# Optimization experiments

Measured on AMD Instinct MI355X. Metric: run time of the kernel, lower is better.

## Reference

```python
import jax, jax.numpy as jnp
import numpy as np

B, C, L = 8, 2048, 256          # batch, seq (EEG channels), feature length
E = 3 * L                        # embed_dim = 768 (fused QKV width)
H = 4                            # attention heads
D = E // (3 * H)                 # head_dim = 64
SCALE = 8.0                      # hardcoded in the module (== sqrt(D) here)


def _layer_norm(x, gamma, beta, eps=1e-5):
    mu = jnp.mean(x, axis=-1, keepdims=True)
    var = jnp.var(x, axis=-1, keepdims=True)
    return (x - mu) * jax.lax.rsqrt(var + eps) * gamma + beta


def setup_inputs() -> dict:
    key = jax.random.key(0)
    ks = jax.random.split(key, 5)
    x = jax.random.normal(ks[0], (B, C, L), dtype=jnp.float32)
    # layers_1: Linear(L -> E) + LayerNorm(E)
    W1 = jax.random.normal(ks[1], (L, E), dtype=jnp.float32) / np.sqrt(L)
    b1 = jnp.zeros((E,), dtype=jnp.float32)
    g1 = jnp.ones((E,), dtype=jnp.float32)
    beta1 = jnp.zeros((E,), dtype=jnp.float32)
    # layers_2: Linear(L -> L) + LayerNorm(L)
    W2 = jax.random.normal(ks[2], (L, L), dtype=jnp.float32) / np.sqrt(L)
    b2 = jnp.zeros((L,), dtype=jnp.float32)
    g2 = jnp.ones((L,), dtype=jnp.float32)
    beta2 = jnp.zeros((L,), dtype=jnp.float32)
    return {"x": x, "W1": W1, "b1": b1, "g1": g1, "beta1": beta1,
            "W2": W2, "b2": b2, "g2": g2, "beta2": beta2}


def reference(x, W1, b1, g1, beta1, W2, b2, g2, beta2):
    b, c, _ = x.shape
    # layers_1 (dropout is identity in eval mode)
    y = _layer_norm(x @ W1 + b1, g1, beta1)                     # [b, c, E]
    qkv = y.reshape(b, c, 3, H, D).transpose(2, 0, 3, 1, 4)     # [3, b, H, c, D]
    q, k, v = qkv[0], qkv[1], qkv[2]
    attn = jax.nn.softmax(jnp.einsum('bhqd,bhkd->bhqk', q, k) / SCALE, axis=-1)
    o = jnp.einsum('bhqk,bhkd->bhqd', attn, v)                  # [b, H, c, D]
    o = o.transpose(0, 2, 1, 3).reshape(b, c, H * D)            # [b, c, L]
    # layers_2 + residual
    z = _layer_norm(o @ W2 + b2, g2, beta2) + x
    return z
```

## Files before the change

### kernel.cpp

```cpp
#include <hip/hip_runtime.h>
#include <hip/hip_bf16.h>

#define B_ 8
#define C_ 2048
#define L_ 256
#define E_ 768
#define H_ 4
#define D_ 64
#define M_ (B_*C_)

typedef __attribute__((ext_vector_type(8))) short short8v;
typedef __attribute__((ext_vector_type(4))) short short4v;
typedef __attribute__((ext_vector_type(4))) float f32x4;

__device__ __forceinline__ short f2bf(float f) {
  union { float f; unsigned u; } v; v.f = f;
  unsigned r = v.u + 0x7FFFu + ((v.u >> 16) & 1u);
  return (short)(r >> 16);
}
__device__ __forceinline__ float bf2f(short s) {
  union { unsigned u; float f; } v; v.u = ((unsigned)(unsigned short)s) << 16;
  return v.f;
}
__device__ __forceinline__ unsigned cvtpk(float a, float b) {
  unsigned r;
  asm("v_cvt_pk_bf16_f32 %0, %1, %2" : "=v"(r) : "v"(a), "v"(b));
  return r;
}
__device__ __forceinline__ float exp2x(float x) {
  float r;
  asm("v_exp_f32 %0, %1" : "=v"(r) : "v"(x));
  return r;
}

__device__ __forceinline__ void gll16(const void* g, void* l) {
  __builtin_amdgcn_global_load_lds(
      (const __attribute__((address_space(1))) unsigned int*)g,
      (__attribute__((address_space(3))) unsigned int*)l, 16, 0, 0);
}

__global__ __launch_bounds__(256) void transpose_w_kernel(const float* __restrict__ W,
                                                          short* __restrict__ Wt,
                                                          int K, int N) {
  __shared__ float ld[32][33];
  const int k0 = blockIdx.x * 32, n0 = blockIdx.y * 32;
  const int tx = threadIdx.x & 31, ty = threadIdx.x >> 5;
  #pragma unroll
  for (int j = 0; j < 4; ++j)
    ld[ty + j*8][tx] = W[(size_t)(k0 + ty + j*8) * N + n0 + tx];
  __syncthreads();
  const int r  = threadIdx.x >> 3;
  const int c0 = (threadIdx.x & 7) * 4;
  short4v o;
  o[0]=f2bf(ld[c0+0][r]); o[1]=f2bf(ld[c0+1][r]);
  o[2]=f2bf(ld[c0+2][r]); o[3]=f2bf(ld[c0+3][r]);
  *(short4v*)(Wt + (size_t)(n0 + r) * K + k0 + c0) = o;
}

__global__ __launch_bounds__(256) void gemm1_mfma_kernel(
    const float* __restrict__ x, const short* __restrict__ W1t,
    const float* __restrict__ b1, short* __restrict__ y1) {
  __shared__ short As[128*72];
  __shared__ short Bs[128*72];
  const int tid = threadIdx.x;
  const int w = tid >> 6, l = tid & 63, lo = l & 15, hi = l >> 4;
  const int wr = w >> 1, wc = w & 1;
  const int m0 = blockIdx.x * 128, n0 = blockIdx.y * 128;

  f32x4 acc[4][4];
  #pragma unroll
  for (int m = 0; m < 4; ++m)
    #pragma unroll
    for (int n = 0; n < 4; ++n) acc[m][n] = (f32x4){0.f,0.f,0.f,0.f};

  for (int kt = 0; kt < 4; ++kt) {
    __syncthreads();
    #pragma unroll
    for (int i = 0; i < 4; ++i) {
      int id = tid + i * 256;
      int row = id >> 3, k8 = (id & 7) * 8;
      const float* ap = x + (size_t)(m0 + row) * 256 + kt*64 + k8;
      float4 a0 = ((const float4*)ap)[0], a1 = ((const float4*)ap)[1];
      uint4 pk;
      pk.x = cvtpk(a0.x, a0.y); pk.y = cvtpk(a0.z, a0.w);
      pk.z = cvtpk(a1.x, a1.y); pk.w = cvtpk(a1.z, a1.w);
      *(uint4*)&As[row*72 + k8] = pk;
      *(short8v*)&Bs[row*72 + k8] =
          *(const short8v*)(W1t + (size_t)(n0 + row) * 256 + kt*64 + k8);
    }
    __syncthreads();
    #pragma unroll
    for (int kk = 0; kk < 2; ++kk) {
      short8v af[4], bf[4];
      #pragma unroll
      for (int m = 0; m < 4; ++m)
        af[m] = *(short8v*)&As[(wr*64 + m*16 + lo)*72 + kk*32 + hi*8];
      #pragma unroll
      for (int n = 0; n < 4; ++n)
        bf[n] = *(short8v*)&Bs[(wc*64 + n*16 + lo)*72 + kk*32 + hi*8];
      #pragma unroll
      for (int m = 0; m < 4; ++m)
        #pragma unroll
        for (int n = 0; n < 4; ++n)
          acc[m][n] = __builtin_amdgcn_mfma_f32_16x16x32_bf16(af[m], bf[n], acc[m][n], 0,0,0);
    }
  }

  float bb[4];
  #pragma unroll
  for (int n = 0; n < 4; ++n) bb[n] = b1[n0 + wc*64 + n*16 + lo];
  #pragma unroll
  for (int m = 0; m < 4; ++m) {
    const int gr = m0 + wr*64 + m*16 + hi*4;
    #pragma unroll
    for (int r = 0; r < 4; ++r) {
      short* yp = y1 + (size_t)(gr + r) * E_ + n0 + wc*64;
      #pragma unroll
      for (int n = 0; n < 4; ++n)
        yp[n*16 + lo] = f2bf(acc[m][n][r] + bb[n]);
    }
  }
}

__global__ __launch_bounds__(256) void ln1_kernel(
    const short* __restrict__ y1, const float* __restrict__ g1,
    const float* __restrict__ be1,
    short* __restrict__ Qg, short* __restrict__ Kg, short* __restrict__ Vtg) {
  __shared__ float mu_s[64], rs_s[64];
  __shared__ short Vlds[64][264];
  const int tid = threadIdx.x;
  const int w = tid >> 6, l = tid & 63;
  const int b = blockIdx.x >> 5;
  const int c0 = (blockIdx.x & 31) * 64;
  const size_t rowbase = (size_t)b * C_ + c0;

  for (int rr = w*16; rr < w*16 + 16; ++rr) {
    const short* yr = y1 + (rowbase + rr) * E_ + l * 12;
    float s = 0.f, s2 = 0.f;
    #pragma unroll
    for (int j = 0; j < 3; ++j) {
      short4v v = *(const short4v*)(yr + j*4);
      #pragma unroll
      for (int t = 0; t < 4; ++t) { float f = bf2f(v[t]); s += f; s2 += f*f; }
    }
    #pragma unroll
    for (int off = 1; off < 64; off <<= 1) {
      s  += __shfl_xor(s, off);
      s2 += __shfl_xor(s2, off);
    }
    if (l == 0) {
      float mu = s * (1.f / E_);
      float var = s2 * (1.f / E_) - mu * mu;
      mu_s[rr] = mu;
      rs_s[rr] = rsqrtf(var + 1e-5f);
    }
  }
  __syncthreads();

  {
    const int chunk = tid & 63, e0 = chunk * 8;
    float gg[8], ee[8];
    #pragma unroll
    for (int j = 0; j < 8; ++j) { gg[j] = g1[e0+j]; ee[j] = be1[e0+j]; }
    const int isQ = (e0 < 256);
    const int eb  = isQ ? e0 : e0 - 256;
    const int h = eb >> 6, d0 = eb & 63;
    short* dstQ = Qg + ((size_t)(b*H_ + h) * C_ + c0) * D_ + d0;
    short* dstK = Kg + ((size_t)(b*H_ + h) * C_ + c0) * D_;
    const float qs = isQ ? 0.18033688011f : 1.f;
    for (int rg = 0; rg < 16; ++rg) {
      int rr = rg*4 + (tid >> 6);
      short8v v = *(const short8v*)(y1 + (rowbase + rr) * E_ + e0);
      float mu = mu_s[rr], rs = rs_s[rr];
      short8v o;
      #pragma unroll
      for (int j = 0; j < 8; ++j)
        o[j] = f2bf(((bf2f(v[j]) - mu) * rs * gg[j] + ee[j]) * qs);
      if (isQ) *(short8v*)(dstQ + (size_t)rr * D_) = o;
      else     *(short8v*)(dstK + (size_t)rr * D_ + ((((d0>>3) ^ (rr&7)) << 3))) = o;
    }
  }
  {
    const int chunk = tid & 31, e0 = 512 + chunk * 8;
    float gg[8], ee[8];
    #pragma unroll
    for (int j = 0; j < 8; ++j) { gg[j] = g1[e0+j]; ee[j] = be1[e0+j]; }
    for (int rg = 0; rg < 8; ++rg) {
      int rr = rg*8 + (tid >> 5);
      short8v v = *(const short8v*)(y1 + (rowbase + rr) * E_ + e0);
      float mu = mu_s[rr], rs = rs_s[rr];
      short8v o;
      #pragma unroll
      for (int j = 0; j < 8; ++j)
        o[j] = f2bf((bf2f(v[j]) - mu) * rs * gg[j] + ee[j]);
      *(short8v*)&Vlds[rr][chunk * 8] = o;
    }
  }
  __syncthreads();
  {
    const int h = tid >> 6, d = tid & 63;
    short* dst = Vtg + ((size_t)(b*H_ + h) * D_ + d) * C_ + c0;
    #pragma unroll
    for (int c8 = 0; c8 < 8; ++c8) {
      short8v vv;
      #pragma unroll
      for (int j = 0; j < 8; ++j) vv[j] = Vlds[c8*8 + j][tid];
      *(short8v*)(dst + ((c8 ^ (d&7)) << 3)) = vv;
    }
  }
}

__global__ __launch_bounds__(512, 4) void attn_mfma_kernel(
    const short* __restrict__ Qg, const short* __restrict__ Kg,
    const short* __restrict__ Vtg, short* __restrict__ ob) {
  __shared__ short Ks[3][4096];
  __shared__ short Vs[3][4096];
  __shared__ short Ps[8][1024];
  const int tid = threadIdx.x;
  const int w  = tid >> 6;
  const int l  = tid & 63, lo = l & 15, hi = l >> 4;
  const int sw = lo & 7;
  const int bh = blockIdx.x, qt = blockIdx.y;
  const size_t hd = (size_t)bh * (C_ * D_);
  const int q0 = qt * 128 + w * 16;

  const short8v bq0 = *(const short8v*)(Qg + hd + (size_t)(q0+lo)*D_ + hi*8);
  const short8v bq1 = *(const short8v*)(Qg + hd + (size_t)(q0+lo)*D_ + 32 + hi*8);

  short8v ones;
  #pragma unroll
  for (int j = 0; j < 8; ++j) ones[j] = (short)0x3F80;

  const short* Ktile = Kg + hd;
  const short* Vrow  = Vtg + hd;
  const int kOff = w*512 + l*8;
  const size_t vOff = (size_t)(w*8 + (l>>3)) * C_ + (l&7)*8;

  f32x4 Oacc[4] = {{0,0,0,0},{0,0,0,0},{0,0,0,0},{0,0,0,0}};
  f32x4 Lacc = {0.f, 0.f, 0.f, 0.f};
  const f32x4 zero4 = {0.f, 0.f, 0.f, 0.f};
  short* Pw = &Ps[w][0];

  gll16(Ktile + kOff, &Ks[0][w*512]);
  gll16(Vrow + vOff,  &Vs[0][w*512]);

  int cur = 0, nxt = 1;
  for (int kt = 0; kt < 32; ++kt) {
    asm volatile("s_waitcnt vmcnt(0)" ::: "memory");
    __builtin_amdgcn_s_barrier();
    if (kt != 31) {
      const short* kn = Ktile + (size_t)(kt+1) * 4096;
      const short* vn = Vrow  + (size_t)(kt+1) * 64;
      gll16(kn + kOff, &Ks[nxt][w*512]);
      gll16(vn + vOff, &Vs[nxt][w*512]);
    }
    const short* Kc = &Ks[cur][0];
    const short* Vc = &Vs[cur][0];

    f32x4 st[4];
    __builtin_amdgcn_s_setprio(1);
    #pragma unroll
    for (int mt = 0; mt < 4; ++mt) {
      short8v ka = *(const short8v*)&Kc[(mt*16 + lo)*64 + ((hi ^ sw) << 3)];
      short8v kb = *(const short8v*)&Kc[(mt*16 + lo)*64 + (((4 + hi) ^ sw) << 3)];
      f32x4 z = __builtin_amdgcn_mfma_f32_16x16x32_bf16(ka, bq0, zero4, 0, 0, 0);
      st[mt]  = __builtin_amdgcn_mfma_f32_16x16x32_bf16(kb, bq1, z, 0, 0, 0);
    }
    __builtin_amdgcn_s_setprio(0);

    float ps[16];
    #pragma unroll
    for (int mt = 0; mt < 4; ++mt)
      #pragma unroll
      for (int r = 0; r < 4; ++r)
        ps[mt*4 + r] = exp2x(st[mt][r]);

    #pragma unroll
    for (int mt = 0; mt < 4; ++mt) {
      uint2 pk;
      pk.x = cvtpk(ps[mt*4+0], ps[mt*4+1]);
      pk.y = cvtpk(ps[mt*4+2], ps[mt*4+3]);
      *(uint2*)&Pw[lo*64 + ((((mt<<1) + (hi>>1)) ^ sw) << 3) + ((hi&1) << 2)] = pk;
    }
    asm volatile("s_waitcnt lgkmcnt(0)" ::: "memory");

    short8v pa0 = *(short8v*)&Pw[lo*64 + ((hi ^ sw) << 3)];
    short8v pa1 = *(short8v*)&Pw[lo*64 + (((4 + hi) ^ sw) << 3)];
    __builtin_amdgcn_s_setprio(1);
    Lacc = __builtin_amdgcn_mfma_f32_16x16x32_bf16(pa0, ones, Lacc, 0, 0, 0);
    Lacc = __builtin_amdgcn_mfma_f32_16x16x32_bf16(pa1, ones, Lacc, 0, 0, 0);
    #pragma unroll
    for (int nt = 0; nt < 4; ++nt) {
      short8v vb0 = *(const short8v*)&Vc[(nt*16 + lo)*64 + ((hi ^ sw) << 3)];
      short8v vb1 = *(const short8v*)&Vc[(nt*16 + lo)*64 + (((4 + hi) ^ sw) << 3)];
      Oacc[nt] = __builtin_amdgcn_mfma_f32_16x16x32_bf16(pa0, vb0, Oacc[nt], 0,0,0);
      Oacc[nt] = __builtin_amdgcn_mfma_f32_16x16x32_bf16(pa1, vb1, Oacc[nt], 0,0,0);
    }
    __builtin_amdgcn_s_setprio(0);
    cur = nxt;
    nxt = (nxt == 2) ? 0 : nxt + 1;
  }

  float invL[4];
  #pragma unroll
  for (int r = 0; r < 4; ++r) invL[r] = 1.f / Lacc[r];
  const int b = bh >> 2, h = bh & 3;
  short* obp = ob + ((size_t)b * C_ + q0) * L_ + h * D_;
  #pragma unroll
  for (int nt = 0; nt < 4; ++nt)
    #pragma unroll
    for (int r = 0; r < 4; ++r)
      obp[(hi*4 + r) * L_ + nt*16 + lo] = f2bf(Oacc[nt][r] * invL[r]);
}

__global__ __launch_bounds__(256) void gemm2_ln_mfma_kernel(
    const short* __restrict__ ob, const short* __restrict__ W2t,
    const float* __restrict__ b2, const float* __restrict__ g2,
    const float* __restrict__ be2, const float* __restrict__ x,
    float* __restrict__ out) {
  __shared__ short As[64*72];
  __shared__ short Bs[256*72];
  __shared__ float2 red[2][2][32];
  const int tid = threadIdx.x;
  const int w = tid >> 6, l = tid & 63, lo = l & 15, hi = l >> 4;
  const int wr = w >> 1, wc = w & 1;
  const int m0 = blockIdx.x * 64;

  f32x4 acc[2][8];
  #pragma unroll
  for (int m = 0; m < 2; ++m)
    #pragma unroll
    for (int n = 0; n < 8; ++n) acc[m][n] = (f32x4){0.f,0.f,0.f,0.f};

  for (int kt = 0; kt < 4; ++kt) {
    __syncthreads();
    #pragma unroll
    for (int i = 0; i < 2; ++i) {
      int id = tid + i * 256;
      int row = id >> 3, k8 = (id & 7) * 8;
      *(short8v*)&As[row*72 + k8] =
          *(const short8v*)(ob + (size_t)(m0 + row) * 256 + kt*64 + k8);
    }
    #pragma unroll
    for (int i = 0; i < 8; ++i) {
      int id = tid + i * 256;
      int row = id >> 3, k8 = (id & 7) * 8;
      *(short8v*)&Bs[row*72 + k8] =
          *(const short8v*)(W2t + (size_t)row * 256 + kt*64 + k8);
    }
    __syncthreads();
    #pragma unroll
    for (int kk = 0; kk < 2; ++kk) {
      short8v af[2], bf[8];
      #pragma unroll
      for (int m = 0; m < 2; ++m)
        af[m] = *(short8v*)&As[(wr*32 + m*16 + lo)*72 + kk*32 + hi*8];
      #pragma unroll
      for (int n = 0; n < 8; ++n)
        bf[n] = *(short8v*)&Bs[(wc*128 + n*16 + lo)*72 + kk*32 + hi*8];
      #pragma unroll
      for (int m = 0; m < 2; ++m)
        #pragma unroll
        for (int n = 0; n < 8; ++n)
          acc[m][n] = __builtin_amdgcn_mfma_f32_16x16x32_bf16(af[m], bf[n], acc[m][n], 0,0,0);
    }
  }

  float bb[8], gg[8], ee[8];
  #pragma unroll
  for (int n = 0; n < 8; ++n) {
    int col = wc*128 + n*16 + lo;
    bb[n] = b2[col]; gg[n] = g2[col]; ee[n] = be2[col];
  }
  float ps[2][4], pq[2][4];
  #pragma unroll
  for (int m = 0; m < 2; ++m)
    #pragma unroll
    for (int r = 0; r < 4; ++r) {
      float s = 0.f, s2 = 0.f;
      #pragma unroll
      for (int n = 0; n < 8; ++n) {
        float v = acc[m][n][r] + bb[n];
        acc[m][n][r] = v;
        s += v; s2 += v*v;
      }
      ps[m][r] = s; pq[m][r] = s2;
    }
  #pragma unroll
  for (int off = 1; off < 16; off <<= 1)
    #pragma unroll
    for (int m = 0; m < 2; ++m)
      #pragma unroll
      for (int r = 0; r < 4; ++r) {
        ps[m][r] += __shfl_xor(ps[m][r], off);
        pq[m][r] += __shfl_xor(pq[m][r], off);
      }
  if (lo == 0)
    #pragma unroll
    for (int m = 0; m < 2; ++m)
      #pragma unroll
      for (int r = 0; r < 4; ++r)
        red[wr][wc][m*16 + hi*4 + r] = make_float2(ps[m][r], pq[m][r]);
  __syncthreads();

  #pragma unroll
  for (int m = 0; m < 2; ++m)
    #pragma unroll
    for (int r = 0; r < 4; ++r) {
      float2 t0 = red[wr][0][m*16 + hi*4 + r];
      float2 t1 = red[wr][1][m*16 + hi*4 + r];
      float s = t0.x + t1.x, s2 = t0.y + t1.y;
      float mu  = s * (1.f / L_);
      float var = s2 * (1.f / L_) - mu * mu;
      float rs  = rsqrtf(var + 1e-5f);
      const int grow = m0 + wr*32 + m*16 + hi*4 + r;
      const float* xr = x + (size_t)grow * L_ + wc*128;
      float* orow = out + (size_t)grow * L_ + wc*128;
      #pragma unroll
      for (int n = 0; n < 8; ++n)
        orow[n*16 + lo] = (acc[m][n][r] - mu) * rs * gg[n] + ee[n] + xr[n*16 + lo];
    }
}

extern "C" void kernel_launch(void* const* d_in, const int* in_sizes, int n_in,
                              void* d_out, int out_size, void* d_ws, size_t ws_size,
                              hipStream_t stream) {
  const float* x   = (const float*)d_in[0];
  const float* W1  = (const float*)d_in[1];
  const float* b1  = (const float*)d_in[2];
  const float* g1  = (const float*)d_in[3];
  const float* be1 = (const float*)d_in[4];
  const float* W2  = (const float*)d_in[5];
  const float* b2  = (const float*)d_in[6];
  const float* g2  = (const float*)d_in[7];
  const float* be2 = (const float*)d_in[8];
  float* out = (float*)d_out;

  const size_t HDSZ = (size_t)B_ * H_ * C_ * D_;
  short* W1t = (short*)d_ws;
  short* W2t = W1t + (size_t)L_ * E_;
  short* y1  = W2t + (size_t)L_ * L_;
  short* Qg  = y1  + (size_t)M_ * E_;
  short* Kg  = Qg  + HDSZ;
  short* Vtg = Kg  + HDSZ;
  short* obm = Vtg + HDSZ;

  transpose_w_kernel<<<dim3(8, 24), 256, 0, stream>>>(W1, W1t, L_, E_);
  transpose_w_kernel<<<dim3(8, 8),  256, 0, stream>>>(W2, W2t, L_, L_);
  gemm1_mfma_kernel<<<dim3(M_ / 128, E_ / 128), 256, 0, stream>>>(x, W1t, b1, y1);
  ln1_kernel<<<M_ / 64, 256, 0, stream>>>(y1, g1, be1, Qg, Kg, Vtg);
  attn_mfma_kernel<<<dim3(32, C_ / 128), 512, 0, stream>>>(Qg, Kg, Vtg, obm);
  gemm2_ln_mfma_kernel<<<M_ / 64, 256, 0, stream>>>(obm, W2t, b2, g2, be2, x, out);
}
```

Baseline: 106.5 us.

## Process two 16-row query tiles per wave in attention to reuse K/V fragments

Cuts the attention block from 8 to 4 waves, and each wave now handles 32 query rows as two 16-row MFMA tiles that share the same K and V fragment loads from LDS. This halves LDS reads of K/V per query row and gives more independent MFMAs per wave, at the cost of higher register pressure. Each wave also issues twice as many global-to-LDS copies, and launch bounds drop to 256 threads with min 2 blocks, which may reduce occupancy.

```diff
diff --git a/kernel.cpp b/kernel.cpp
--- a/kernel.cpp
+++ b/kernel.cpp
@@ -210,22 +210,24 @@
   }
 }
 
-__global__ __launch_bounds__(512, 4) void attn_mfma_kernel(
+__global__ __launch_bounds__(256, 2) void attn_mfma_kernel(
     const short* __restrict__ Qg, const short* __restrict__ Kg,
     const short* __restrict__ Vtg, short* __restrict__ ob) {
   __shared__ short Ks[3][4096];
   __shared__ short Vs[3][4096];
-  __shared__ short Ps[8][1024];
+  __shared__ short Ps[4][2048];
   const int tid = threadIdx.x;
   const int w  = tid >> 6;
   const int l  = tid & 63, lo = l & 15, hi = l >> 4;
   const int sw = lo & 7;
   const int bh = blockIdx.x, qt = blockIdx.y;
   const size_t hd = (size_t)bh * (C_ * D_);
-  const int q0 = qt * 128 + w * 16;
-
-  const short8v bq0 = *(const short8v*)(Qg + hd + (size_t)(q0+lo)*D_ + hi*8);
-  const short8v bq1 = *(const short8v*)(Qg + hd + (size_t)(q0+lo)*D_ + 32 + hi*8);
+  const int q0 = qt * 128 + w * 32;
+
+  const short8v bqA0 = *(const short8v*)(Qg + hd + (size_t)(q0+lo)*D_ + hi*8);
+  const short8v bqA1 = *(const short8v*)(Qg + hd + (size_t)(q0+lo)*D_ + 32 + hi*8);
+  const short8v bqB0 = *(const short8v*)(Qg + hd + (size_t)(q0+16+lo)*D_ + hi*8);
+  const short8v bqB1 = *(const short8v*)(Qg + hd + (size_t)(q0+16+lo)*D_ + 32 + hi*8);
 
   short8v ones;
   #pragma unroll
@@ -233,16 +235,22 @@
 
   const short* Ktile = Kg + hd;
   const short* Vrow  = Vtg + hd;
-  const int kOff = w*512 + l*8;
-  const size_t vOff = (size_t)(w*8 + (l>>3)) * C_ + (l&7)*8;
-
-  f32x4 Oacc[4] = {{0,0,0,0},{0,0,0,0},{0,0,0,0},{0,0,0,0}};
-  f32x4 Lacc = {0.f, 0.f, 0.f, 0.f};
+  const int segA = w*2, segB = segA + 1;
+  const int kOffA = segA*512 + l*8, kOffB = segB*512 + l*8;
+  const size_t vOffA = (size_t)(segA*8 + (l>>3)) * C_ + (l&7)*8;
+  const size_t vOffB = (size_t)(segB*8 + (l>>3)) * C_ + (l&7)*8;
+
+  f32x4 OaccA[4] = {{0,0,0,0},{0,0,0,0},{0,0,0,0},{0,0,0,0}};
+  f32x4 OaccB[4] = {{0,0,0,0},{0,0,0,0},{0,0,0,0},{0,0,0,0}};
+  f32x4 LaccA = {0.f,0.f,0.f,0.f}, LaccB = {0.f,0.f,0.f,0.f};
   const f32x4 zero4 = {0.f, 0.f, 0.f, 0.f};
-  short* Pw = &Ps[w][0];
-
-  gll16(Ktile + kOff, &Ks[0][w*512]);
-  gll16(Vrow + vOff,  &Vs[0][w*512]);
+  short* PwA = &Ps[w][0];
+  short* PwB = &Ps[w][1024];
+
+  gll16(Ktile + kOffA, &Ks[0][segA*512]);
+  gll16(Ktile + kOffB, &Ks[0][segB*512]);
+  gll16(Vrow + vOffA,  &Vs[0][segA*512]);
+  gll16(Vrow + vOffB,  &Vs[0][segB*512]);
 
   int cur = 0, nxt = 1;
   for (int kt = 0; kt < 32; ++kt) {
@@ -251,66 +259,85 @@
     if (kt != 31) {
       const short* kn = Ktile + (size_t)(kt+1) * 4096;
       const short* vn = Vrow  + (size_t)(kt+1) * 64;
-      gll16(kn + kOff, &Ks[nxt][w*512]);
-      gll16(vn + vOff, &Vs[nxt][w*512]);
+      gll16(kn + kOffA, &Ks[nxt][segA*512]);
+      gll16(kn + kOffB, &Ks[nxt][segB*512]);
+      gll16(vn + vOffA, &Vs[nxt][segA*512]);
+      gll16(vn + vOffB, &Vs[nxt][segB*512]);
     }
     const short* Kc = &Ks[cur][0];
     const short* Vc = &Vs[cur][0];
 
-    f32x4 st[4];
+    f32x4 stA[4], stB[4];
     __builtin_amdgcn_s_setprio(1);
     #pragma unroll
     for (int mt = 0; mt < 4; ++mt) {
       short8v ka = *(const short8v*)&Kc[(mt*16 + lo)*64 + ((hi ^ sw) << 3)];
       short8v kb = *(const short8v*)&Kc[(mt*16 + lo)*64 + (((4 + hi) ^ sw) << 3)];
-      f32x4 z = __builtin_amdgcn_mfma_f32_16x16x32_bf16(ka, bq0, zero4, 0, 0, 0);
-      st[mt]  = __builtin_amdgcn_mfma_f32_16x16x32_bf16(kb, bq1, z, 0, 0, 0);
+      f32x4 zA = __builtin_amdgcn_mfma_f32_16x16x32_bf16(ka, bqA0, zero4, 0, 0, 0);
+      stA[mt]  = __builtin_amdgcn_mfma_f32_16x16x32_bf16(kb, bqA1, zA, 0, 0, 0);
+      f32x4 zB = __builtin_amdgcn_mfma_f32_16x16x32_bf16(ka, bqB0, zero4, 0, 0, 0);
+      stB[mt]  = __builtin_amdgcn_mfma_f32_16x16x32_bf16(kb, bqB1, zB, 0, 0, 0);
     }
     __builtin_amdgcn_s_setprio(0);
 
-    float ps[16];
+    float psA[16], psB[16];
     #pragma unroll
     for (int mt = 0; mt < 4; ++mt)
       #pragma unroll
-      for (int r = 0; r < 4; ++r)
-        ps[mt*4 + r] = exp2x(st[mt][r]);
+      for (int r = 0; r < 4; ++r) {
+        psA[mt*4 + r] = exp2x(stA[mt][r]);
+        psB[mt*4 + r] = exp2x(stB[mt][r]);
+      }
 
     #pragma unroll
     for (int mt = 0; mt < 4; ++mt) {
-      uint2 pk;
-      pk.x = cvtpk(ps[mt*4+0], ps[mt*4+1]);
-      pk.y = cvtpk(ps[mt*4+2], ps[mt*4+3]);
-      *(uint2*)&Pw[lo*64 + ((((mt<<1) + (hi>>1)) ^ sw) << 3) + ((hi&1) << 2)] = pk;
+      const int off = lo*64 + ((((mt<<1) + (hi>>1)) ^ sw) << 3) + ((hi&1) << 2);
+      uint2 pkA, pkB;
+      pkA.x = cvtpk(psA[mt*4+0], psA[mt*4+1]);
+      pkA.y = cvtpk(psA[mt*4+2], psA[mt*4+3]);
+      pkB.x = cvtpk(psB[mt*4+0], psB[mt*4+1]);
+      pkB.y = cvtpk(psB[mt*4+2], psB[mt*4+3]);
+      *(uint2*)&PwA[off] = pkA;
+      *(uint2*)&PwB[off] = pkB;
     }
     asm volatile("s_waitcnt lgkmcnt(0)" ::: "memory");
 
-    short8v pa0 = *(short8v*)&Pw[lo*64 + ((hi ^ sw) << 3)];
-    short8v pa1 = *(short8v*)&Pw[lo*64 + (((4 + hi) ^ sw) << 3)];
+    short8v paA0 = *(short8v*)&PwA[lo*64 + ((hi ^ sw) << 3)];
+    short8v paA1 = *(short8v*)&PwA[lo*64 + (((4 + hi) ^ sw) << 3)];
+    short8v paB0 = *(short8v*)&PwB[lo*64 + ((hi ^ sw) << 3)];
+    short8v paB1 = *(short8v*)&PwB[lo*64 + (((4 + hi) ^ sw) << 3)];
     __builtin_amdgcn_s_setprio(1);
-    Lacc = __builtin_amdgcn_mfma_f32_16x16x32_bf16(pa0, ones, Lacc, 0, 0, 0);
-    Lacc = __builtin_amdgcn_mfma_f32_16x16x32_bf16(pa1, ones, Lacc, 0, 0, 0);
+    LaccA = __builtin_amdgcn_mfma_f32_16x16x32_bf16(paA0, ones, LaccA, 0, 0, 0);
+    LaccA = __builtin_amdgcn_mfma_f32_16x16x32_bf16(paA1, ones, LaccA, 0, 0, 0);
+    LaccB = __builtin_amdgcn_mfma_f32_16x16x32_bf16(paB0, ones, LaccB, 0, 0, 0);
+    LaccB = __builtin_amdgcn_mfma_f32_16x16x32_bf16(paB1, ones, LaccB, 0, 0, 0);
     #pragma unroll
     for (int nt = 0; nt < 4; ++nt) {
       short8v vb0 = *(const short8v*)&Vc[(nt*16 + lo)*64 + ((hi ^ sw) << 3)];
       short8v vb1 = *(const short8v*)&Vc[(nt*16 + lo)*64 + (((4 + hi) ^ sw) << 3)];
-      Oacc[nt] = __builtin_amdgcn_mfma_f32_16x16x32_bf16(pa0, vb0, Oacc[nt], 0,0,0);
-      Oacc[nt] = __builtin_amdgcn_mfma_f32_16x16x32_bf16(pa1, vb1, Oacc[nt], 0,0,0);
+      OaccA[nt] = __builtin_amdgcn_mfma_f32_16x16x32_bf16(paA0, vb0, OaccA[nt], 0,0,0);
+      OaccA[nt] = __builtin_amdgcn_mfma_f32_16x16x32_bf16(paA1, vb1, OaccA[nt], 0,0,0);
+      OaccB[nt] = __builtin_amdgcn_mfma_f32_16x16x32_bf16(paB0, vb0, OaccB[nt], 0,0,0);
+      OaccB[nt] = __builtin_amdgcn_mfma_f32_16x16x32_bf16(paB1, vb1, OaccB[nt], 0,0,0);
     }
     __builtin_amdgcn_s_setprio(0);
     cur = nxt;
     nxt = (nxt == 2) ? 0 : nxt + 1;
   }
 
-  float invL[4];
-  #pragma unroll
-  for (int r = 0; r < 4; ++r) invL[r] = 1.f / Lacc[r];
+  float invA[4], invB[4];
+  #pragma unroll
+  for (int r = 0; r < 4; ++r) { invA[r] = 1.f / LaccA[r]; invB[r] = 1.f / LaccB[r]; }
   const int b = bh >> 2, h = bh & 3;
-  short* obp = ob + ((size_t)b * C_ + q0) * L_ + h * D_;
+  short* obpA = ob + ((size_t)b * C_ + q0) * L_ + h * D_;
+  short* obpB = ob + ((size_t)b * C_ + q0 + 16) * L_ + h * D_;
   #pragma unroll
   for (int nt = 0; nt < 4; ++nt)
     #pragma unroll
-    for (int r = 0; r < 4; ++r)
-      obp[(hi*4 + r) * L_ + nt*16 + lo] = f2bf(Oacc[nt][r] * invL[r]);
+    for (int r = 0; r < 4; ++r) {
+      obpA[(hi*4 + r) * L_ + nt*16 + lo] = f2bf(OaccA[nt][r] * invA[r]);
+      obpB[(hi*4 + r) * L_ + nt*16 + lo] = f2bf(OaccB[nt][r] * invB[r]);
+    }
 }
 
 __global__ __launch_bounds__(256) void gemm2_ln_mfma_kernel(
@@ -449,6 +476,6 @@
   transpose_w_kernel<<<dim3(8, 8),  256, 0, stream>>>(W2, W2t, L_, L_);
   gemm1_mfma_kernel<<<dim3(M_ / 128, E_ / 128), 256, 0, stream>>>(x, W1t, b1, y1);
   ln1_kernel<<<M_ / 64, 256, 0, stream>>>(y1, g1, be1, Qg, Kg, Vtg);
-  attn_mfma_kernel<<<dim3(32, C_ / 128), 512, 0, stream>>>(Qg, Kg, Vtg, obm);
+  attn_mfma_kernel<<<dim3(32, C_ / 128), 256, 0, stream>>>(Qg, Kg, Vtg, obm);
   gemm2_ln_mfma_kernel<<<M_ / 64, 256, 0, stream>>>(obm, W2t, b2, g2, be2, x, out);
 }
```

Result: no change. 108.6 us (+1.9%).

## Fuse first GEMM with LayerNorm and QKV scatter into one kernel

Applied to the files above, without the earlier changes.

Replaces the separate GEMM1 and LN1 kernels with one kernel. Each block computes 32 full rows of the 768-wide projection, reduces the LayerNorm statistics across waves in shared memory, and writes the swizzled Q, K and transposed V layouts straight from registers. This removes the bf16 y1 intermediate round trip through global memory and one launch. In exchange, W1t is read directly from global memory per wave without LDS staging, and the Q/K stores become scattered 2-byte writes.

```diff
diff --git a/kernel.cpp b/kernel.cpp
--- a/kernel.cpp
+++ b/kernel.cpp
@@ -17,10 +17,6 @@
   union { float f; unsigned u; } v; v.f = f;
   unsigned r = v.u + 0x7FFFu + ((v.u >> 16) & 1u);
   return (short)(r >> 16);
-}
-__device__ __forceinline__ float bf2f(short s) {
-  union { unsigned u; float f; } v; v.u = ((unsigned)(unsigned short)s) << 16;
-  return v.f;
 }
 __device__ __forceinline__ unsigned cvtpk(float a, float b) {
   unsigned r;
@@ -57,155 +53,136 @@
   *(short4v*)(Wt + (size_t)(n0 + r) * K + k0 + c0) = o;
 }
 
-__global__ __launch_bounds__(256) void gemm1_mfma_kernel(
+__global__ __launch_bounds__(512, 2) void gemm1_ln_fused_kernel(
     const float* __restrict__ x, const short* __restrict__ W1t,
-    const float* __restrict__ b1, short* __restrict__ y1) {
-  __shared__ short As[128*72];
-  __shared__ short Bs[128*72];
+    const float* __restrict__ b1, const float* __restrict__ g1,
+    const float* __restrict__ be1,
+    short* __restrict__ Qg, short* __restrict__ Kg, short* __restrict__ Vtg) {
+  __shared__ short As[32*264];
+  __shared__ float2 red[8][32];
+  __shared__ float mu_s[32], rs_s[32];
   const int tid = threadIdx.x;
   const int w = tid >> 6, l = tid & 63, lo = l & 15, hi = l >> 4;
-  const int wr = w >> 1, wc = w & 1;
-  const int m0 = blockIdx.x * 128, n0 = blockIdx.y * 128;
-
-  f32x4 acc[4][4];
-  #pragma unroll
-  for (int m = 0; m < 4; ++m)
-    #pragma unroll
-    for (int n = 0; n < 4; ++n) acc[m][n] = (f32x4){0.f,0.f,0.f,0.f};
-
-  for (int kt = 0; kt < 4; ++kt) {
-    __syncthreads();
-    #pragma unroll
-    for (int i = 0; i < 4; ++i) {
-      int id = tid + i * 256;
-      int row = id >> 3, k8 = (id & 7) * 8;
-      const float* ap = x + (size_t)(m0 + row) * 256 + kt*64 + k8;
-      float4 a0 = ((const float4*)ap)[0], a1 = ((const float4*)ap)[1];
-      uint4 pk;
-      pk.x = cvtpk(a0.x, a0.y); pk.y = cvtpk(a0.z, a0.w);
-      pk.z = cvtpk(a1.x, a1.y); pk.w = cvtpk(a1.z, a1.w);
-      *(uint4*)&As[row*72 + k8] = pk;
-      *(short8v*)&Bs[row*72 + k8] =
-          *(const short8v*)(W1t + (size_t)(n0 + row) * 256 + kt*64 + k8);
-    }
-    __syncthreads();
+  const int m0 = blockIdx.x * 32;
+  const int b = m0 >> 11, c0 = m0 & (C_ - 1);
+  const int nbase = w * 96;
+
+  {
+    const int row = tid >> 4, cc = (tid & 15) * 16;
+    const float* ap = x + (size_t)(m0 + row) * 256 + cc;
+    float4 a0 = ((const float4*)ap)[0], a1 = ((const float4*)ap)[1];
+    float4 a2 = ((const float4*)ap)[2], a3 = ((const float4*)ap)[3];
+    uint4 p0, p1;
+    p0.x = cvtpk(a0.x,a0.y); p0.y = cvtpk(a0.z,a0.w);
+    p0.z = cvtpk(a1.x,a1.y); p0.w = cvtpk(a1.z,a1.w);
+    p1.x = cvtpk(a2.x,a2.y); p1.y = cvtpk(a2.z,a2.w);
+    p1.z = cvtpk(a3.x,a3.y); p1.w = cvtpk(a3.z,a3.w);
+    *(uint4*)&As[row*264 + cc]     = p0;
+    *(uint4*)&As[row*264 + cc + 8] = p1;
+  }
+  __syncthreads();
+
+  f32x4 acc[2][6];
+  #pragma unroll
+  for (int m = 0; m < 2; ++m)
+    #pragma unroll
+    for (int n = 0; n < 6; ++n) acc[m][n] = (f32x4){0.f,0.f,0.f,0.f};
+
+  #pragma unroll
+  for (int kt = 0; kt < 4; ++kt)
     #pragma unroll
     for (int kk = 0; kk < 2; ++kk) {
-      short8v af[4], bf[4];
-      #pragma unroll
-      for (int m = 0; m < 4; ++m)
-        af[m] = *(short8v*)&As[(wr*64 + m*16 + lo)*72 + kk*32 + hi*8];
-      #pragma unroll
-      for (int n = 0; n < 4; ++n)
-        bf[n] = *(short8v*)&Bs[(wc*64 + n*16 + lo)*72 + kk*32 + hi*8];
-      #pragma unroll
-      for (int m = 0; m < 4; ++m)
+      short8v bf[6];
+      #pragma unroll
+      for (int n = 0; n < 6; ++n)
+        bf[n] = *(const short8v*)(W1t + (size_t)(nbase + n*16 + lo) * 256
+                                     + kt*64 + kk*32 + hi*8);
+      short8v af0 = *(short8v*)&As[lo*264      + kt*64 + kk*32 + hi*8];
+      short8v af1 = *(short8v*)&As[(16+lo)*264 + kt*64 + kk*32 + hi*8];
+      #pragma unroll
+      for (int n = 0; n < 6; ++n) {
+        acc[0][n] = __builtin_amdgcn_mfma_f32_16x16x32_bf16(af0, bf[n], acc[0][n], 0,0,0);
+        acc[1][n] = __builtin_amdgcn_mfma_f32_16x16x32_bf16(af1, bf[n], acc[1][n], 0,0,0);
+      }
+    }
+
+  float bb[6], ggv[6], eev[6];
+  #pragma unroll
+  for (int n = 0; n < 6; ++n) {
+    int col = nbase + n*16 + lo;
+    bb[n] = b1[col]; ggv[n] = g1[col]; eev[n] = be1[col];
+  }
+  #pragma unroll
+  for (int m = 0; m < 2; ++m)
+    #pragma unroll
+    for (int r = 0; r < 4; ++r) {
+      float s = 0.f, s2 = 0.f;
+      #pragma unroll
+      for (int n = 0; n < 6; ++n) {
+        float v = acc[m][n][r] + bb[n];
+        acc[m][n][r] = v;
+        s += v; s2 += v*v;
+      }
+      #pragma unroll
+      for (int off = 1; off < 16; off <<= 1) {
+        s  += __shfl_xor(s, off);
+        s2 += __shfl_xor(s2, off);
+      }
+      if (lo == 0) red[w][m*16 + hi*4 + r] = make_float2(s, s2);
+    }
+  __syncthreads();
+  if (tid < 32) {
+    float s = 0.f, s2 = 0.f;
+    #pragma unroll
+    for (int wv = 0; wv < 8; ++wv) { s += red[wv][tid].x; s2 += red[wv][tid].y; }
+    float mu = s * (1.f / E_);
+    float var = s2 * (1.f / E_) - mu * mu;
+    mu_s[tid] = mu;
+    rs_s[tid] = rsqrtf(var + 1e-5f);
+  }
+  __syncthreads();
+
+  const float qs = 0.18033688011f;
+  #pragma unroll
+  for (int m = 0; m < 2; ++m) {
+    float mu4[4], rs4[4];
+    #pragma unroll
+    for (int r = 0; r < 4; ++r) {
+      int row = m*16 + hi*4 + r;
+      mu4[r] = mu_s[row]; rs4[r] = rs_s[row];
+    }
+    const int cbase = c0 + m*16 + hi*4;
+    #pragma unroll
+    for (int n = 0; n < 6; ++n) {
+      const int e0 = nbase + n*16 + lo;
+      float vals[4];
+      #pragma unroll
+      for (int r = 0; r < 4; ++r)
+        vals[r] = (acc[m][n][r] - mu4[r]) * rs4[r] * ggv[n] + eev[n];
+      if (e0 < 256) {
+        const int h = e0 >> 6, d = e0 & 63;
+        short* base = Qg + ((size_t)(b*H_ + h) * C_) * D_ + d;
         #pragma unroll
-        for (int n = 0; n < 4; ++n)
-          acc[m][n] = __builtin_amdgcn_mfma_f32_16x16x32_bf16(af[m], bf[n], acc[m][n], 0,0,0);
-    }
-  }
-
-  float bb[4];
-  #pragma unroll
-  for (int n = 0; n < 4; ++n) bb[n] = b1[n0 + wc*64 + n*16 + lo];
-  #pragma unroll
-  for (int m = 0; m < 4; ++m) {
-    const int gr = m0 + wr*64 + m*16 + hi*4;
-    #pragma unroll
-    for (int r = 0; r < 4; ++r) {
-      short* yp = y1 + (size_t)(gr + r) * E_ + n0 + wc*64;
-      #pragma unroll
-      for (int n = 0; n < 4; ++n)
-        yp[n*16 + lo] = f2bf(acc[m][n][r] + bb[n]);
-    }
-  }
-}
-
-__global__ __launch_bounds__(256) void ln1_kernel(
-    const short* __restrict__ y1, const float* __restrict__ g1,
-    const float* __restrict__ be1,
-    short* __restrict__ Qg, short* __restrict__ Kg, short* __restrict__ Vtg) {
-  __shared__ float mu_s[64], rs_s[64];
-  __shared__ short Vlds[64][264];
-  const int tid = threadIdx.x;
-  const int w = tid >> 6, l = tid & 63;
-  const int b = blockIdx.x >> 5;
-  const int c0 = (blockIdx.x & 31) * 64;
-  const size_t rowbase = (size_t)b * C_ + c0;
-
-  for (int rr = w*16; rr < w*16 + 16; ++rr) {
-    const short* yr = y1 + (rowbase + rr) * E_ + l * 12;
-    float s = 0.f, s2 = 0.f;
-    #pragma unroll
-    for (int j = 0; j < 3; ++j) {
-      short4v v = *(const short4v*)(yr + j*4);
-      #pragma unroll
-      for (int t = 0; t < 4; ++t) { float f = bf2f(v[t]); s += f; s2 += f*f; }
-    }
-    #pragma unroll
-    for (int off = 1; off < 64; off <<= 1) {
-      s  += __shfl_xor(s, off);
-      s2 += __shfl_xor(s2, off);
-    }
-    if (l == 0) {
-      float mu = s * (1.f / E_);
-      float var = s2 * (1.f / E_) - mu * mu;
-      mu_s[rr] = mu;
-      rs_s[rr] = rsqrtf(var + 1e-5f);
-    }
-  }
-  __syncthreads();
-
-  {
-    const int chunk = tid & 63, e0 = chunk * 8;
-    float gg[8], ee[8];
-    #pragma unroll
-    for (int j = 0; j < 8; ++j) { gg[j] = g1[e0+j]; ee[j] = be1[e0+j]; }
-    const int isQ = (e0 < 256);
-    const int eb  = isQ ? e0 : e0 - 256;
-    const int h = eb >> 6, d0 = eb & 63;
-    short* dstQ = Qg + ((size_t)(b*H_ + h) * C_ + c0) * D_ + d0;
-    short* dstK = Kg + ((size_t)(b*H_ + h) * C_ + c0) * D_;
-    const float qs = isQ ? 0.18033688011f : 1.f;
-    for (int rg = 0; rg < 16; ++rg) {
-      int rr = rg*4 + (tid >> 6);
-      short8v v = *(const short8v*)(y1 + (rowbase + rr) * E_ + e0);
-      float mu = mu_s[rr], rs = rs_s[rr];
-      short8v o;
-      #pragma unroll
-      for (int j = 0; j < 8; ++j)
-        o[j] = f2bf(((bf2f(v[j]) - mu) * rs * gg[j] + ee[j]) * qs);
-      if (isQ) *(short8v*)(dstQ + (size_t)rr * D_) = o;
-      else     *(short8v*)(dstK + (size_t)rr * D_ + ((((d0>>3) ^ (rr&7)) << 3))) = o;
-    }
-  }
-  {
-    const int chunk = tid & 31, e0 = 512 + chunk * 8;
-    float gg[8], ee[8];
-    #pragma unroll
-    for (int j = 0; j < 8; ++j) { gg[j] = g1[e0+j]; ee[j] = be1[e0+j]; }
-    for (int rg = 0; rg < 8; ++rg) {
-      int rr = rg*8 + (tid >> 5);
-      short8v v = *(const short8v*)(y1 + (rowbase + rr) * E_ + e0);
-      float mu = mu_s[rr], rs = rs_s[rr];
-      short8v o;
-      #pragma unroll
-      for (int j = 0; j < 8; ++j)
-        o[j] = f2bf((bf2f(v[j]) - mu) * rs * gg[j] + ee[j]);
-      *(short8v*)&Vlds[rr][chunk * 8] = o;
-    }
-  }
-  __syncthreads();
-  {
-    const int h = tid >> 6, d = tid & 63;
-    short* dst = Vtg + ((size_t)(b*H_ + h) * D_ + d) * C_ + c0;
-    #pragma unroll
-    for (int c8 = 0; c8 < 8; ++c8) {
-      short8v vv;
-      #pragma unroll
-      for (int j = 0; j < 8; ++j) vv[j] = Vlds[c8*8 + j][tid];
-      *(short8v*)(dst + ((c8 ^ (d&7)) << 3)) = vv;
+        for (int r = 0; r < 4; ++r)
+          base[(size_t)(cbase + r) * D_] = f2bf(vals[r] * qs);
+      } else if (e0 < 512) {
+        const int eb = e0 - 256, h = eb >> 6, d = eb & 63;
+        short* base = Kg + ((size_t)(b*H_ + h) * C_) * D_;
+        #pragma unroll
+        for (int r = 0; r < 4; ++r) {
+          int c = cbase + r;
+          base[(size_t)c * D_ + (((d>>3) ^ (c&7)) << 3) + (d&7)] = f2bf(vals[r]);
+        }
+      } else {
+        const int eb = e0 - 512, h = eb >> 6, d = eb & 63;
+        short4v pk;
+        #pragma unroll
+        for (int r = 0; r < 4; ++r) pk[r] = f2bf(vals[r]);
+        const int c = cbase;
+        size_t off = ((size_t)(b*H_ + h) * D_ + d) * C_ + (c & ~63)
+                   + ((((c & 63) >> 3) ^ (d & 7)) << 3) + (c & 7);
+        *(short4v*)(Vtg + off) = pk;
+      }
     }
   }
 }
@@ -439,16 +416,14 @@
   const size_t HDSZ = (size_t)B_ * H_ * C_ * D_;
   short* W1t = (short*)d_ws;
   short* W2t = W1t + (size_t)L_ * E_;
-  short* y1  = W2t + (size_t)L_ * L_;
-  short* Qg  = y1  + (size_t)M_ * E_;
+  short* Qg  = W2t + (size_t)L_ * L_;
   short* Kg  = Qg  + HDSZ;
   short* Vtg = Kg  + HDSZ;
   short* obm = Vtg + HDSZ;
 
   transpose_w_kernel<<<dim3(8, 24), 256, 0, stream>>>(W1, W1t, L_, E_);
   transpose_w_kernel<<<dim3(8, 8),  256, 0, stream>>>(W2, W2t, L_, L_);
-  gemm1_mfma_kernel<<<dim3(M_ / 128, E_ / 128), 256, 0, stream>>>(x, W1t, b1, y1);
-  ln1_kernel<<<M_ / 64, 256, 0, stream>>>(y1, g1, be1, Qg, Kg, Vtg);
+  gemm1_ln_fused_kernel<<<M_ / 32, 512, 0, stream>>>(x, W1t, b1, g1, be1, Qg, Kg, Vtg);
   attn_mfma_kernel<<<dim3(32, C_ / 128), 512, 0, stream>>>(Qg, Kg, Vtg, obm);
   gemm2_ln_mfma_kernel<<<M_ / 64, 256, 0, stream>>>(obm, W2t, b2, g2, be2, x, out);
 }
```

Result: faster. 102.8 us (-3.5%).

## Permute K layout to keep P in registers, retile gemm2, merge weight transposes

Applied to the files above, without the earlier changes.

K rows are written in a permuted order inside each 32-row group, so the MFMA score output layout matches the A-operand layout for the P·V MFMA. This lets the attention kernel pack P straight into registers and drop the per-wave LDS round trip and its wait. The gemm2+LayerNorm kernel is retiled to 32-row blocks: the whole A tile goes into LDS once, W2 fragments are read directly from global/L2, and there are more blocks and fewer barriers. The two weight-transpose launches are merged into one. The risk is correctness: the K permutation has to match the MFMA lane mapping exactly.

```diff
diff --git a/kernel.cpp b/kernel.cpp
--- a/kernel.cpp
+++ b/kernel.cpp
@@ -12,6 +12,7 @@
 typedef __attribute__((ext_vector_type(8))) short short8v;
 typedef __attribute__((ext_vector_type(4))) short short4v;
 typedef __attribute__((ext_vector_type(4))) float f32x4;
+typedef __attribute__((ext_vector_type(4))) unsigned uint4v;
 
 __device__ __forceinline__ short f2bf(float f) {
   union { float f; unsigned u; } v; v.f = f;
@@ -39,11 +40,15 @@
       (__attribute__((address_space(3))) unsigned int*)l, 16, 0, 0);
 }
 
-__global__ __launch_bounds__(256) void transpose_w_kernel(const float* __restrict__ W,
-                                                          short* __restrict__ Wt,
-                                                          int K, int N) {
+__global__ __launch_bounds__(256) void transpose_w_kernel(
+    const float* __restrict__ W1, short* __restrict__ W1t,
+    const float* __restrict__ W2, short* __restrict__ W2t) {
   __shared__ float ld[32][33];
-  const int k0 = blockIdx.x * 32, n0 = blockIdx.y * 32;
+  const int isW1 = blockIdx.y < 24;
+  const float* W = isW1 ? W1 : W2;
+  short* Wt = isW1 ? W1t : W2t;
+  const int N = isW1 ? E_ : L_;
+  const int k0 = blockIdx.x * 32, n0 = (isW1 ? blockIdx.y : blockIdx.y - 24) * 32;
   const int tx = threadIdx.x & 31, ty = threadIdx.x >> 5;
   #pragma unroll
   for (int j = 0; j < 4; ++j)
@@ -54,7 +59,7 @@
   short4v o;
   o[0]=f2bf(ld[c0+0][r]); o[1]=f2bf(ld[c0+1][r]);
   o[2]=f2bf(ld[c0+2][r]); o[3]=f2bf(ld[c0+3][r]);
-  *(short4v*)(Wt + (size_t)(n0 + r) * K + k0 + c0) = o;
+  *(short4v*)(Wt + (size_t)(n0 + r) * 256 + k0 + c0) = o;
 }
 
 __global__ __launch_bounds__(256) void gemm1_mfma_kernel(
@@ -176,8 +181,14 @@
       #pragma unroll
       for (int j = 0; j < 8; ++j)
         o[j] = f2bf(((bf2f(v[j]) - mu) * rs * gg[j] + ee[j]) * qs);
-      if (isQ) *(short8v*)(dstQ + (size_t)rr * D_) = o;
-      else     *(short8v*)(dstK + (size_t)rr * D_ + ((((d0>>3) ^ (rr&7)) << 3))) = o;
+      if (isQ) {
+        *(short8v*)(dstQ + (size_t)rr * D_) = o;
+      } else {
+        int a5 = rr & 31;
+        int p5 = (((a5 >> 2) & 1) << 4) | (((a5 >> 3) & 3) << 2) | (a5 & 3);
+        int cs = (rr & ~31) | p5;
+        *(short8v*)(dstK + (size_t)cs * D_ + (((d0>>3) ^ (cs&7)) << 3)) = o;
+      }
     }
   }
   {
@@ -215,7 +226,6 @@
     const short* __restrict__ Vtg, short* __restrict__ ob) {
   __shared__ short Ks[3][4096];
   __shared__ short Vs[3][4096];
-  __shared__ short Ps[8][1024];
   const int tid = threadIdx.x;
   const int w  = tid >> 6;
   const int l  = tid & 63, lo = l & 15, hi = l >> 4;
@@ -239,7 +249,6 @@
   f32x4 Oacc[4] = {{0,0,0,0},{0,0,0,0},{0,0,0,0},{0,0,0,0}};
   f32x4 Lacc = {0.f, 0.f, 0.f, 0.f};
   const f32x4 zero4 = {0.f, 0.f, 0.f, 0.f};
-  short* Pw = &Ps[w][0];
 
   gll16(Ktile + kOff, &Ks[0][w*512]);
   gll16(Vrow + vOff,  &Vs[0][w*512]);
@@ -274,18 +283,13 @@
       #pragma unroll
       for (int r = 0; r < 4; ++r)
         ps[mt*4 + r] = exp2x(st[mt][r]);
-
-    #pragma unroll
-    for (int mt = 0; mt < 4; ++mt) {
-      uint2 pk;
-      pk.x = cvtpk(ps[mt*4+0], ps[mt*4+1]);
-      pk.y = cvtpk(ps[mt*4+2], ps[mt*4+3]);
-      *(uint2*)&Pw[lo*64 + ((((mt<<1) + (hi>>1)) ^ sw) << 3) + ((hi&1) << 2)] = pk;
-    }
-    asm volatile("s_waitcnt lgkmcnt(0)" ::: "memory");
-
-    short8v pa0 = *(short8v*)&Pw[lo*64 + ((hi ^ sw) << 3)];
-    short8v pa1 = *(short8v*)&Pw[lo*64 + (((4 + hi) ^ sw) << 3)];
+    uint4v up0 = { cvtpk(ps[0], ps[1]),  cvtpk(ps[2], ps[3]),
+                   cvtpk(ps[4], ps[5]),  cvtpk(ps[6], ps[7]) };
+    uint4v up1 = { cvtpk(ps[8], ps[9]),  cvtpk(ps[10], ps[11]),
+                   cvtpk(ps[12], ps[13]), cvtpk(ps[14], ps[15]) };
+    short8v pa0 = __builtin_bit_cast(short8v, up0);
+    short8v pa1 = __builtin_bit_cast(short8v, up1);
+
     __builtin_amdgcn_s_setprio(1);
     Lacc = __builtin_amdgcn_mfma_f32_16x16x32_bf16(pa0, ones, Lacc, 0, 0, 0);
     Lacc = __builtin_amdgcn_mfma_f32_16x16x32_bf16(pa1, ones, Lacc, 0, 0, 0);
@@ -313,113 +317,107 @@
       obp[(hi*4 + r) * L_ + nt*16 + lo] = f2bf(Oacc[nt][r] * invL[r]);
 }
 
-__global__ __launch_bounds__(256) void gemm2_ln_mfma_kernel(
+__global__ __launch_bounds__(256, 4) void gemm2_ln_mfma_kernel(
     const short* __restrict__ ob, const short* __restrict__ W2t,
     const float* __restrict__ b2, const float* __restrict__ g2,
     const float* __restrict__ be2, const float* __restrict__ x,
     float* __restrict__ out) {
-  __shared__ short As[64*72];
-  __shared__ short Bs[256*72];
-  __shared__ float2 red[2][2][32];
+  __shared__ short As[32*264];
+  __shared__ float2 red[4][32];
+  __shared__ float mu_s[32], rs_s[32];
   const int tid = threadIdx.x;
   const int w = tid >> 6, l = tid & 63, lo = l & 15, hi = l >> 4;
-  const int wr = w >> 1, wc = w & 1;
-  const int m0 = blockIdx.x * 64;
-
-  f32x4 acc[2][8];
+  const int m0 = blockIdx.x * 32;
+  const int nbase = w * 64;
+
+  #pragma unroll
+  for (int i = 0; i < 4; ++i) {
+    int id = tid + i * 256;
+    int row = id >> 5, c8 = (id & 31) * 8;
+    *(short8v*)&As[row*264 + c8] =
+        *(const short8v*)(ob + (size_t)(m0 + row) * 256 + c8);
+  }
+  __syncthreads();
+
+  f32x4 acc[2][4];
   #pragma unroll
   for (int m = 0; m < 2; ++m)
     #pragma unroll
-    for (int n = 0; n < 8; ++n) acc[m][n] = (f32x4){0.f,0.f,0.f,0.f};
-
-  for (int kt = 0; kt < 4; ++kt) {
-    __syncthreads();
-    #pragma unroll
-    for (int i = 0; i < 2; ++i) {
-      int id = tid + i * 256;
-      int row = id >> 3, k8 = (id & 7) * 8;
-      *(short8v*)&As[row*72 + k8] =
-          *(const short8v*)(ob + (size_t)(m0 + row) * 256 + kt*64 + k8);
-    }
-    #pragma unroll
-    for (int i = 0; i < 8; ++i) {
-      int id = tid + i * 256;
-      int row = id >> 3, k8 = (id & 7) * 8;
-      *(short8v*)&Bs[row*72 + k8] =
-          *(const short8v*)(W2t + (size_t)row * 256 + kt*64 + k8);
-    }
-    __syncthreads();
+    for (int n = 0; n < 4; ++n) acc[m][n] = (f32x4){0.f,0.f,0.f,0.f};
+
+  #pragma unroll
+  for (int kt = 0; kt < 4; ++kt)
     #pragma unroll
     for (int kk = 0; kk < 2; ++kk) {
-      short8v af[2], bf[8];
-      #pragma unroll
-      for (int m = 0; m < 2; ++m)
-        af[m] = *(short8v*)&As[(wr*32 + m*16 + lo)*72 + kk*32 + hi*8];
-      #pragma unroll
-      for (int n = 0; n < 8; ++n)
-        bf[n] = *(short8v*)&Bs[(wc*128 + n*16 + lo)*72 + kk*32 + hi*8];
-      #pragma unroll
-      for (int m = 0; m < 2; ++m)
-        #pragma unroll
-        for (int n = 0; n < 8; ++n)
-          acc[m][n] = __builtin_amdgcn_mfma_f32_16x16x32_bf16(af[m], bf[n], acc[m][n], 0,0,0);
-    }
-  }
-
-  float bb[8], gg[8], ee[8];
-  #pragma unroll
-  for (int n = 0; n < 8; ++n) {
-    int col = wc*128 + n*16 + lo;
+      short8v bf[4];
+      #pragma unroll
+      for (int n = 0; n < 4; ++n)
+        bf[n] = *(const short8v*)(W2t + (size_t)(nbase + n*16 + lo) * 256
+                                     + kt*64 + kk*32 + hi*8);
+      short8v af0 = *(short8v*)&As[lo*264      + kt*64 + kk*32 + hi*8];
+      short8v af1 = *(short8v*)&As[(16+lo)*264 + kt*64 + kk*32 + hi*8];
+      #pragma unroll
+      for (int n = 0; n < 4; ++n) {
+        acc[0][n] = __builtin_amdgcn_mfma_f32_16x16x32_bf16(af0, bf[n], acc[0][n], 0,0,0);
+        acc[1][n] = __builtin_amdgcn_mfma_f32_16x16x32_bf16(af1, bf[n], acc[1][n], 0,0,0);
+      }
+    }
+
+  float bb[4], gg[4], ee[4];
+  #pragma unroll
+  for (int n = 0; n < 4; ++n) {
+    int col = nbase + n*16 + lo;
     bb[n] = b2[col]; gg[n] = g2[col]; ee[n] = be2[col];
   }
-  float ps[2][4], pq[2][4];
   #pragma unroll
   for (int m = 0; m < 2; ++m)
     #pragma unroll
     for (int r = 0; r < 4; ++r) {
       float s = 0.f, s2 = 0.f;
       #pragma unroll
-      for (int n = 0; n < 8; ++n) {
+      for (int n = 0; n < 4; ++n) {
         float v = acc[m][n][r] + bb[n];
         acc[m][n][r] = v;
         s += v; s2 += v*v;
       }
-      ps[m][r] = s; pq[m][r] = s2;
-    }
-  #pragma unroll
-  for (int off = 1; off < 16; off <<= 1)
-    #pragma unroll
-    for (int m = 0; m < 2; ++m)
-      #pragma unroll
-      for (int r = 0; r < 4; ++r) {
-        ps[m][r] += __shfl_xor(ps[m][r], off);
-        pq[m][r] += __shfl_xor(pq[m][r], off);
+      #pragma unroll
+      for (int off = 1; off < 16; off <<= 1) {
+        s  += __shfl_xor(s, off);
+        s2 += __shfl_xor(s2, off);
       }
-  if (lo == 0)
-    #pragma unroll
-    for (int m = 0; m < 2; ++m)
-      #pragma unroll
-      for (int r = 0; r < 4; ++r)
-        red[wr][wc][m*16 + hi*4 + r] = make_float2(ps[m][r], pq[m][r]);
-  __syncthreads();
-
-  #pragma unroll
-  for (int m = 0; m < 2; ++m)
+      if (lo == 0) red[w][m*16 + hi*4 + r] = make_float2(s, s2);
+    }
+  __syncthreads();
+  if (tid < 32) {
+    float s = 0.f, s2 = 0.f;
+    #pragma unroll
+    for (int wv = 0; wv < 4; ++wv) { s += red[wv][tid].x; s2 += red[wv][tid].y; }
+    float mu = s * (1.f / L_);
+    float var = s2 * (1.f / L_) - mu * mu;
+    mu_s[tid] = mu;
+    rs_s[tid] = rsqrtf(var + 1e-5f);
+  }
+  __syncthreads();
+
+  #pragma unroll
+  for (int m = 0; m < 2; ++m) {
+    float mu4[4], rs4[4];
     #pragma unroll
     for (int r = 0; r < 4; ++r) {
-      float2 t0 = red[wr][0][m*16 + hi*4 + r];
-      float2 t1 = red[wr][1][m*16 + hi*4 + r];
-      float s = t0.x + t1.x, s2 = t0.y + t1.y;
-      float mu  = s * (1.f / L_);
-      float var = s2 * (1.f / L_) - mu * mu;
-      float rs  = rsqrtf(var + 1e-5f);
-      const int grow = m0 + wr*32 + m*16 + hi*4 + r;
-      const float* xr = x + (size_t)grow * L_ + wc*128;
-      float* orow = out + (size_t)grow * L_ + wc*128;
-      #pragma unroll
-      for (int n = 0; n < 8; ++n)
-        orow[n*16 + lo] = (acc[m][n][r] - mu) * rs * gg[n] + ee[n] + xr[n*16 + lo];
-    }
+      int row = m*16 + hi*4 + r;
+      mu4[r] = mu_s[row]; rs4[r] = rs_s[row];
+    }
+    #pragma unroll
+    for (int r = 0; r < 4; ++r) {
+      const int grow = m0 + m*16 + hi*4 + r;
+      const float* xr = x + (size_t)grow * L_ + nbase;
+      float* orow = out + (size_t)grow * L_ + nbase;
+      #pragma unroll
+      for (int n = 0; n < 4; ++n)
+        orow[n*16 + lo] = (acc[m][n][r] - mu4[r]) * rs4[r] * gg[n] + ee[n]
+                        + xr[n*16 + lo];
+    }
+  }
 }
 
 extern "C" void kernel_launch(void* const* d_in, const int* in_sizes, int n_in,
@@ -445,10 +443,9 @@
   short* Vtg = Kg  + HDSZ;
   short* obm = Vtg + HDSZ;
 
-  transpose_w_kernel<<<dim3(8, 24), 256, 0, stream>>>(W1, W1t, L_, E_);
-  transpose_w_kernel<<<dim3(8, 8),  256, 0, stream>>>(W2, W2t, L_, L_);
+  transpose_w_kernel<<<dim3(8, 32), 256, 0, stream>>>(W1, W1t, W2, W2t);
   gemm1_mfma_kernel<<<dim3(M_ / 128, E_ / 128), 256, 0, stream>>>(x, W1t, b1, y1);
   ln1_kernel<<<M_ / 64, 256, 0, stream>>>(y1, g1, be1, Qg, Kg, Vtg);
   attn_mfma_kernel<<<dim3(32, C_ / 128), 512, 0, stream>>>(Qg, Kg, Vtg, obm);
-  gemm2_ln_mfma_kernel<<<M_ / 64, 256, 0, stream>>>(obm, W2t, b2, g2, be2, x, out);
-}
+  gemm2_ln_mfma_kernel<<<M_ / 32, 256, 0, stream>>>(obm, W2t, b2, g2, be2, x, out);
+}
```

New measurement: 103.8 us. -2.6%, faster.
